# Performance work log

Measured on AMD Instinct MI355X. Metric: run time of the kernel, lower is better.

Reference implementation:

```python
import jax, jax.numpy as jnp
import numpy as np

MARGIN = 1.0
EPS = 1e-6  # torch F.pairwise_distance default eps, added elementwise to (x - y)
NEG_INF = -1e30
POS_INF = 1e30


def _pairwise_dist_matrix(e):
    # D[i,j] = || e_i - e_j + EPS ||_2, expanded so we never materialize [B,B,D]:
    # ||d + eps||^2 = ||d||^2 + 2*eps*sum(d) + Dfeat*eps^2,  d = e_i - e_j
    sq = jnp.sum(e * e, axis=1)          # [B]
    s = jnp.sum(e, axis=1)               # [B]
    d2 = (sq[:, None] + sq[None, :] - 2.0 * (e @ e.T)
          + 2.0 * EPS * (s[:, None] - s[None, :])
          + e.shape[1] * (EPS * EPS))
    return jnp.sqrt(jnp.maximum(d2, 0.0))  # [B,B]


def _pdist(x, y):
    # F.pairwise_distance(p=2): ||x - y + eps||
    return jnp.sqrt(jnp.sum(jnp.square(x - y + EPS), axis=-1))


def setup_inputs() -> dict:
    B, D = 4096, 128
    key = jax.random.key(0)
    k1, k2, k3, k4 = jax.random.split(key, 4)
    embedding = jax.random.normal(k1, (B, D), dtype=jnp.float32)
    # label space == batch, each label appears exactly once in the batch
    target_idx = jax.random.permutation(k2, B).astype(jnp.int32)
    positive_idxs = jax.random.bernoulli(k3, 0.02, (B, B))  # [B, L] label-space mask
    negative_idxs = jax.random.bernoulli(k4, 0.5, (B, B))
    return {"embedding": embedding, "target_idx": target_idx,
            "positive_idxs": positive_idxs, "negative_idxs": negative_idxs}


def reference(embedding, target_idx, positive_idxs, negative_idxs):
    # Mining happens under no_grad in the original module.
    dm = jax.lax.stop_gradient(_pairwise_dist_matrix(embedding))  # [B,B]
    # batch j is a positive/negative candidate for anchor i iff its label is flagged
    pos_mask = positive_idxs[:, target_idx]  # [B,B] bool
    neg_mask = negative_idxs[:, target_idx]
    pos_idx = jnp.argmax(jnp.where(pos_mask, dm, NEG_INF), axis=1)  # hardest positive
    neg_idx = jnp.argmin(jnp.where(neg_mask, dm, POS_INF), axis=1)  # hardest negative
    valid = jnp.any(pos_mask, axis=1) & jnp.any(neg_mask, axis=1)
    a = embedding
    p = embedding[pos_idx]
    n = embedding[neg_idx]
    ap = _pdist(a, p)
    an = _pdist(a, n)
    pn = _pdist(p, n)
    loss = jax.nn.relu(ap - jnp.minimum(an, pn) + MARGIN)
    w = valid.astype(loss.dtype)
    return jnp.sum(loss * w) / jnp.maximum(jnp.sum(w), 1.0)
```

## Files before the change

kernel.cpp:

```cpp
#include <hip/hip_runtime.h>
#include <stdint.h>

#define BN 4096
#define DD 128
#define EPSF 1e-6f
#define MARGINF 1.0f

typedef unsigned long long ull;
typedef unsigned short ushort;
typedef short short8 __attribute__((ext_vector_type(8)));
typedef float f32x4 __attribute__((ext_vector_type(4)));

__device__ __forceinline__ unsigned int ord_f32(float f) {
    unsigned int u = __float_as_uint(f);
    return (u & 0x80000000u) ? ~u : (u | 0x80000000u);
}
__device__ __forceinline__ ushort bf16_rne(float x) {
    unsigned int u = __float_as_uint(x);
    return (ushort)((u + 0x7FFFu + ((u >> 16) & 1u)) >> 16);
}

__global__ void k_prep(const float* __restrict__ e, const int* __restrict__ tidx,
                       float* __restrict__ rjp, unsigned int* __restrict__ jn,
                       ull* __restrict__ pk, ull* __restrict__ nk,
                       unsigned int* __restrict__ ehi, unsigned int* __restrict__ eperm) {
    int w = threadIdx.x >> 6, lane = threadIdx.x & 63;
    int row = blockIdx.x * 4 + w;
    int c = tidx[row];
    float2 v = ((const float2*)(e + (size_t)row * DD))[lane];
    ushort hx = bf16_rne(v.x), hy = bf16_rne(v.y);
    unsigned int packed = (unsigned int)hx | ((unsigned int)hy << 16);
    ehi[row * 64 + lane] = packed;
    eperm[(size_t)c * 64 + lane] = packed;
    float ss = v.x + v.y;
    float qq = v.x * v.x + v.y * v.y;
    #pragma unroll
    for (int off = 32; off > 0; off >>= 1) {
        ss += __shfl_down(ss, off);
        qq += __shfl_down(qq, off);
    }
    if (lane == 0) {
        rjp[c] = qq - 2.0f * EPSF * ss;
        jn[c] = 0xFFFFFFFFu - (unsigned int)row;
        pk[row] = 0ULL; nk[row] = 0ULL;
    }
}

__global__ __launch_bounds__(256, 4)
void k_select(const ushort* __restrict__ ehi, const ushort* __restrict__ eperm,
              const int* __restrict__ pos, const int* __restrict__ neg,
              const float* __restrict__ rjp, const unsigned int* __restrict__ jn,
              ull* __restrict__ pkey, ull* __restrict__ nkey) {
    __shared__ float rjL[1024];
    __shared__ unsigned int jnL[1024];
    __shared__ ull scrp[16 * 4], scrn[16 * 4];

    const int tid = threadIdx.x;
    const int lane = tid & 63, w = tid >> 6;
    const int lrow = lane & 15, quad = lane >> 4;
    const int r0 = blockIdx.x * 16;
    const int c0 = blockIdx.y * 1024;

    #pragma unroll
    for (int k = 0; k < 4; k++) {
        int idx = k * 256 + tid;
        rjL[idx] = rjp[c0 + idx];
        jnL[idx] = jn[c0 + idx];
    }

    short8 a[4];
    #pragma unroll
    for (int ks = 0; ks < 4; ks++)
        a[ks] = *(const short8*)(ehi + (size_t)(r0 + lrow) * DD + ks * 32 + quad * 8);

    __syncthreads();

    ull kp[4] = {0ULL, 0ULL, 0ULL, 0ULL};
    ull kn[4] = {0ULL, 0ULL, 0ULL, 0ULL};

    int pm[2][4], nm[2][4];
    short8 bf[2][4];
    float rjc[2]; unsigned int jni[2];

#define LOADTILE(BUF, JT) do {                                                 \
        const int lcol = (JT) * 64 + w * 16 + lrow;                            \
        rjc[BUF] = rjL[lcol];                                                  \
        jni[BUF] = jnL[lcol];                                                  \
        const int* pp = pos + (size_t)(r0 + quad * 4) * BN + (size_t)(c0 + lcol); \
        const int* np = neg + (size_t)(r0 + quad * 4) * BN + (size_t)(c0 + lcol); \
        _Pragma("unroll")                                                      \
        for (int t = 0; t < 4; t++) {                                          \
            pm[BUF][t] = __builtin_nontemporal_load(pp + (size_t)t * BN);      \
            nm[BUF][t] = __builtin_nontemporal_load(np + (size_t)t * BN);      \
        }                                                                      \
        const ushort* bp = eperm + (size_t)(c0 + lcol) * DD + quad * 8;        \
        _Pragma("unroll")                                                      \
        for (int ks = 0; ks < 4; ks++)                                         \
            bf[BUF][ks] = *(const short8*)(bp + ks * 32);                      \
    } while (0)

    LOADTILE(0, 0);

    #pragma unroll
    for (int jt = 0; jt < 16; jt++) {
        const int cur = jt & 1, nxt = cur ^ 1;
        if (jt < 15) {
            if (nxt == 0) LOADTILE(0, jt + 1); else LOADTILE(1, jt + 1);
        }
        f32x4 acc = (f32x4){0.f, 0.f, 0.f, 0.f};
        #pragma unroll
        for (int ks = 0; ks < 4; ks++)
            acc = __builtin_amdgcn_mfma_f32_16x16x32_bf16(a[ks], bf[cur][ks], acc, 0, 0, 0);
        #pragma unroll
        for (int t = 0; t < 4; t++) {
            float m = rjc[cur] - 2.0f * acc[t];
            unsigned int om = ord_f32(m);
            ull keyp = ((ull)om << 32) | (ull)jni[cur];
            ull keyn = ((ull)(om ^ 0xFFFFFFFFu) << 32) | (ull)jni[cur];
            if (pm[cur][t] != 0 && keyp > kp[t]) kp[t] = keyp;
            if (nm[cur][t] != 0 && keyn > kn[t]) kn[t] = keyn;
        }
    }
#undef LOADTILE

    #pragma unroll
    for (int t = 0; t < 4; t++) {
        #pragma unroll
        for (int off = 8; off > 0; off >>= 1) {
            ull o = __shfl_xor(kp[t], off); if (o > kp[t]) kp[t] = o;
            o = __shfl_xor(kn[t], off);     if (o > kn[t]) kn[t] = o;
        }
        if (lrow == 0) {
            scrp[(quad * 4 + t) * 4 + w] = kp[t];
            scrn[(quad * 4 + t) * 4 + w] = kn[t];
        }
    }
    __syncthreads();
    if (tid < 16) {
        ull xp = 0ULL, xn = 0ULL;
        #pragma unroll
        for (int k = 0; k < 4; k++) {
            ull v = scrp[tid * 4 + k]; if (v > xp) xp = v;
            v = scrn[tid * 4 + k];     if (v > xn) xn = v;
        }
        if (xp) atomicMax(&pkey[r0 + tid], xp);
        if (xn) atomicMax(&nkey[r0 + tid], xn);
    }
}

__global__ void k_loss(const float* __restrict__ e,
                       const ull* __restrict__ pkey, const ull* __restrict__ nkey,
                       float* __restrict__ partials) {
    int w = threadIdx.x >> 6, lane = threadIdx.x & 63;
    int row = blockIdx.x * 4 + w;
    ull pk = pkey[row], nk = nkey[row];
    float loss = 0.0f, wt = 0.0f;
    if (pk != 0ULL && nk != 0ULL) {
        int pi = (int)(0xFFFFFFFFu - (unsigned)(pk & 0xFFFFFFFFu));
        int ni = (int)(0xFFFFFFFFu - (unsigned)(nk & 0xFFFFFFFFu));
        float2 av = ((const float2*)(e + (size_t)row * DD))[lane];
        float2 pv = ((const float2*)(e + (size_t)pi * DD))[lane];
        float2 nv = ((const float2*)(e + (size_t)ni * DD))[lane];
        float dx, dy;
        dx = av.x - pv.x + EPSF; dy = av.y - pv.y + EPSF;
        float ap2 = dx * dx + dy * dy;
        dx = av.x - nv.x + EPSF; dy = av.y - nv.y + EPSF;
        float an2 = dx * dx + dy * dy;
        dx = pv.x - nv.x + EPSF; dy = pv.y - nv.y + EPSF;
        float pn2 = dx * dx + dy * dy;
        #pragma unroll
        for (int off = 32; off > 0; off >>= 1) {
            ap2 += __shfl_down(ap2, off);
            an2 += __shfl_down(an2, off);
            pn2 += __shfl_down(pn2, off);
        }
        if (lane == 0) {
            float ap = sqrtf(ap2), an = sqrtf(an2), pn = sqrtf(pn2);
            loss = fmaxf(ap - fminf(an, pn) + MARGINF, 0.0f);
            wt = 1.0f;
        }
    }
    __shared__ float sl[4], sw[4];
    if (lane == 0) { sl[w] = loss; sw[w] = wt; }
    __syncthreads();
    if (threadIdx.x == 0) {
        partials[blockIdx.x * 2 + 0] = sl[0] + sl[1] + sl[2] + sl[3];
        partials[blockIdx.x * 2 + 1] = sw[0] + sw[1] + sw[2] + sw[3];
    }
}

__global__ void k_final(const float* __restrict__ partials, float* __restrict__ out) {
    int tid = threadIdx.x;
    float L = 0.0f, W = 0.0f;
    for (int i = 0; i < 4; i++) {
        int idx = tid + i * 256;
        L += partials[idx * 2];
        W += partials[idx * 2 + 1];
    }
    #pragma unroll
    for (int off = 32; off > 0; off >>= 1) {
        L += __shfl_down(L, off);
        W += __shfl_down(W, off);
    }
    __shared__ float sl[4], sw[4];
    int w = tid >> 6, lane = tid & 63;
    if (lane == 0) { sl[w] = L; sw[w] = W; }
    __syncthreads();
    if (tid == 0) {
        float Lt = sl[0] + sl[1] + sl[2] + sl[3];
        float Wt = sw[0] + sw[1] + sw[2] + sw[3];
        out[0] = Lt / fmaxf(Wt, 1.0f);
    }
}

extern "C" void kernel_launch(void* const* d_in, const int* in_sizes, int n_in,
                              void* d_out, int out_size, void* d_ws, size_t ws_size,
                              hipStream_t stream) {
    const float* e    = (const float*)d_in[0];
    const int*   tidx = (const int*)d_in[1];
    const int*   pos  = (const int*)d_in[2];
    const int*   neg  = (const int*)d_in[3];
    float* out = (float*)d_out;

    ull* pkey  = (ull*)d_ws;
    ull* nkey  = pkey + BN;
    float* rjp = (float*)(nkey + BN);
    unsigned int* jn = (unsigned int*)(rjp + BN);
    float* partials  = (float*)(jn + BN);
    unsigned int* ehi   = (unsigned int*)(partials + 2048);
    unsigned int* eperm = ehi + (size_t)BN * 64;

    k_prep<<<BN / 4, 256, 0, stream>>>(e, tidx, rjp, jn, pkey, nkey, ehi, eperm);
    dim3 grid(BN / 16, 4);
    k_select<<<grid, 256, 0, stream>>>((const ushort*)ehi, (const ushort*)eperm,
                                       pos, neg, rjp, jn, pkey, nkey);
    k_loss<<<BN / 4, 256, 0, stream>>>(e, pkey, nkey, partials);
    k_final<<<1, 256, 0, stream>>>(partials, out);
}
```

Before: 184.5 us.

## Pack pos/neg int masks into bitmasks in prep kernel before selection

The prep kernel now streams each row of the int32 positive/negative masks with 16-byte nontemporal loads and packs them into 64-bit bitmasks. The selection kernel then reads one bit word per 64 columns instead of scattered int32 loads per element. The aim is better-coalesced mask streaming and fewer loads inside the MFMA loop. The cost is an extra 4 MB write and read, with the path gated on workspace size.

```diff
diff --git a/kernel.cpp b/kernel.cpp
--- a/kernel.cpp
+++ b/kernel.cpp
@@ -10,6 +10,7 @@
 typedef unsigned short ushort;
 typedef short short8 __attribute__((ext_vector_type(8)));
 typedef float f32x4 __attribute__((ext_vector_type(4)));
+typedef int int4v __attribute__((ext_vector_type(4)));
 
 __device__ __forceinline__ unsigned int ord_f32(float f) {
     unsigned int u = __float_as_uint(f);
@@ -20,13 +21,16 @@
     return (ushort)((u + 0x7FFFu + ((u >> 16) & 1u)) >> 16);
 }
 
+template<bool BITS>
 __global__ void k_prep(const float* __restrict__ e, const int* __restrict__ tidx,
+                       const int* __restrict__ pos, const int* __restrict__ neg,
                        float* __restrict__ rjp, unsigned int* __restrict__ jn,
-                       ull* __restrict__ pk, ull* __restrict__ nk,
-                       unsigned int* __restrict__ ehi, unsigned int* __restrict__ eperm) {
-    int w = threadIdx.x >> 6, lane = threadIdx.x & 63;
-    int row = blockIdx.x * 4 + w;
-    int c = tidx[row];
+                       ull* __restrict__ pkey, ull* __restrict__ nkey,
+                       unsigned int* __restrict__ ehi, unsigned int* __restrict__ eperm,
+                       ull* __restrict__ pbits, ull* __restrict__ nbits) {
+    const int w = threadIdx.x >> 6, lane = threadIdx.x & 63;
+    const int row = blockIdx.x * 4 + w;
+    const int c = tidx[row];
     float2 v = ((const float2*)(e + (size_t)row * DD))[lane];
     ushort hx = bf16_rne(v.x), hy = bf16_rne(v.y);
     unsigned int packed = (unsigned int)hx | ((unsigned int)hy << 16);
@@ -42,24 +46,51 @@
     if (lane == 0) {
         rjp[c] = qq - 2.0f * EPSF * ss;
         jn[c] = 0xFFFFFFFFu - (unsigned int)row;
-        pk[row] = 0ULL; nk[row] = 0ULL;
-    }
-}
-
+        pkey[row] = 0ULL; nkey[row] = 0ULL;
+    }
+    if (BITS) {
+        ushort* pb16 = (ushort*)pbits;
+        ushort* nb16 = (ushort*)nbits;
+        const int4v* prow = (const int4v*)(pos + (size_t)row * BN);
+        const int4v* nrow = (const int4v*)(neg + (size_t)row * BN);
+        #pragma unroll
+        for (int seg = 0; seg < 4; seg++) {
+            unsigned int pu = 0, nu = 0;
+            #pragma unroll
+            for (int k = 0; k < 4; k++) {
+                int4v P = __builtin_nontemporal_load(&prow[seg * 256 + lane * 4 + k]);
+                int4v N = __builtin_nontemporal_load(&nrow[seg * 256 + lane * 4 + k]);
+                unsigned int pq = (unsigned int)(P[0] != 0) | ((unsigned int)(P[1] != 0) << 1)
+                                | ((unsigned int)(P[2] != 0) << 2) | ((unsigned int)(P[3] != 0) << 3);
+                unsigned int nq = (unsigned int)(N[0] != 0) | ((unsigned int)(N[1] != 0) << 1)
+                                | ((unsigned int)(N[2] != 0) << 2) | ((unsigned int)(N[3] != 0) << 3);
+                pu |= pq << (4 * k);
+                nu |= nq << (4 * k);
+            }
+            pb16[row * 256 + seg * 64 + lane] = (ushort)pu;
+            nb16[row * 256 + seg * 64 + lane] = (ushort)nu;
+        }
+    }
+}
+
+template<bool BITS>
 __global__ __launch_bounds__(256, 4)
 void k_select(const ushort* __restrict__ ehi, const ushort* __restrict__ eperm,
               const int* __restrict__ pos, const int* __restrict__ neg,
+              const ull* __restrict__ pbits, const ull* __restrict__ nbits,
               const float* __restrict__ rjp, const unsigned int* __restrict__ jn,
               ull* __restrict__ pkey, ull* __restrict__ nkey) {
     __shared__ float rjL[1024];
     __shared__ unsigned int jnL[1024];
-    __shared__ ull scrp[16 * 4], scrn[16 * 4];
+    __shared__ ull scrp[64], scrn[64];
 
     const int tid = threadIdx.x;
     const int lane = tid & 63, w = tid >> 6;
     const int lrow = lane & 15, quad = lane >> 4;
     const int r0 = blockIdx.x * 16;
     const int c0 = blockIdx.y * 1024;
+    const int cb0 = c0 >> 6;
+    const int shft = w * 16 + lrow;
 
     #pragma unroll
     for (int k = 0; k < 4; k++) {
@@ -78,25 +109,36 @@
     ull kp[4] = {0ULL, 0ULL, 0ULL, 0ULL};
     ull kn[4] = {0ULL, 0ULL, 0ULL, 0ULL};
 
+    ull pmw[2][4], nmw[2][4];
     int pm[2][4], nm[2][4];
     short8 bf[2][4];
     float rjc[2]; unsigned int jni[2];
 
-#define LOADTILE(BUF, JT) do {                                                 \
-        const int lcol = (JT) * 64 + w * 16 + lrow;                            \
-        rjc[BUF] = rjL[lcol];                                                  \
-        jni[BUF] = jnL[lcol];                                                  \
-        const int* pp = pos + (size_t)(r0 + quad * 4) * BN + (size_t)(c0 + lcol); \
-        const int* np = neg + (size_t)(r0 + quad * 4) * BN + (size_t)(c0 + lcol); \
-        _Pragma("unroll")                                                      \
-        for (int t = 0; t < 4; t++) {                                          \
-            pm[BUF][t] = __builtin_nontemporal_load(pp + (size_t)t * BN);      \
-            nm[BUF][t] = __builtin_nontemporal_load(np + (size_t)t * BN);      \
-        }                                                                      \
-        const ushort* bp = eperm + (size_t)(c0 + lcol) * DD + quad * 8;        \
-        _Pragma("unroll")                                                      \
-        for (int ks = 0; ks < 4; ks++)                                         \
-            bf[BUF][ks] = *(const short8*)(bp + ks * 32);                      \
+#define LOADTILE(BUF, JT) do {                                                  \
+        const int lcol = (JT) * 64 + shft;                                      \
+        rjc[BUF] = rjL[lcol];                                                   \
+        jni[BUF] = jnL[lcol];                                                   \
+        if (BITS) {                                                             \
+            const ull* pb = pbits + (size_t)(r0 + quad * 4) * 64 + cb0 + (JT);  \
+            const ull* nb = nbits + (size_t)(r0 + quad * 4) * 64 + cb0 + (JT);  \
+            _Pragma("unroll")                                                   \
+            for (int t = 0; t < 4; t++) {                                       \
+                pmw[BUF][t] = pb[(size_t)t * 64];                               \
+                nmw[BUF][t] = nb[(size_t)t * 64];                               \
+            }                                                                   \
+        } else {                                                                \
+            const int* pp = pos + (size_t)(r0 + quad * 4) * BN + (size_t)(c0 + lcol); \
+            const int* np = neg + (size_t)(r0 + quad * 4) * BN + (size_t)(c0 + lcol); \
+            _Pragma("unroll")                                                   \
+            for (int t = 0; t < 4; t++) {                                       \
+                pm[BUF][t] = __builtin_nontemporal_load(pp + (size_t)t * BN);   \
+                nm[BUF][t] = __builtin_nontemporal_load(np + (size_t)t * BN);   \
+            }                                                                   \
+        }                                                                       \
+        const ushort* bp = eperm + (size_t)(c0 + lcol) * DD + quad * 8;         \
+        _Pragma("unroll")                                                       \
+        for (int ks = 0; ks < 4; ks++)                                          \
+            bf[BUF][ks] = *(const short8*)(bp + ks * 32);                       \
     } while (0)
 
     LOADTILE(0, 0);
@@ -117,8 +159,10 @@
             unsigned int om = ord_f32(m);
             ull keyp = ((ull)om << 32) | (ull)jni[cur];
             ull keyn = ((ull)(om ^ 0xFFFFFFFFu) << 32) | (ull)jni[cur];
-            if (pm[cur][t] != 0 && keyp > kp[t]) kp[t] = keyp;
-            if (nm[cur][t] != 0 && keyn > kn[t]) kn[t] = keyn;
+            bool pok = BITS ? (((pmw[cur][t] >> shft) & 1ULL) != 0ULL) : (pm[cur][t] != 0);
+            bool nok = BITS ? (((nmw[cur][t] >> shft) & 1ULL) != 0ULL) : (nm[cur][t] != 0);
+            if (pok && keyp > kp[t]) kp[t] = keyp;
+            if (nok && keyn > kn[t]) kn[t] = keyn;
         }
     }
 #undef LOADTILE
@@ -222,18 +266,33 @@
     const int*   neg  = (const int*)d_in[3];
     float* out = (float*)d_out;
 
-    ull* pkey  = (ull*)d_ws;
-    ull* nkey  = pkey + BN;
-    float* rjp = (float*)(nkey + BN);
-    unsigned int* jn = (unsigned int*)(rjp + BN);
-    float* partials  = (float*)(jn + BN);
-    unsigned int* ehi   = (unsigned int*)(partials + 2048);
-    unsigned int* eperm = ehi + (size_t)BN * 64;
-
-    k_prep<<<BN / 4, 256, 0, stream>>>(e, tidx, rjp, jn, pkey, nkey, ehi, eperm);
+    char* p = (char*)d_ws;
+    ull* pkey  = (ull*)p;                 p += (size_t)BN * 8;
+    ull* nkey  = (ull*)p;                 p += (size_t)BN * 8;
+    float* rjp = (float*)p;               p += (size_t)BN * 4;
+    unsigned int* jn = (unsigned int*)p;  p += (size_t)BN * 4;
+    float* partials = (float*)p;          p += 2048 * 4;
+    unsigned int* ehi = (unsigned int*)p; p += (size_t)BN * 64 * 4;
+    unsigned int* eperm = (unsigned int*)p; p += (size_t)BN * 64 * 4;
+    ull* pbits = (ull*)p;                 p += (size_t)BN * 64 * 8;
+    ull* nbits = (ull*)p;                 p += (size_t)BN * 64 * 8;
+    const size_t need = (size_t)(p - (char*)d_ws);
+    const bool bits = ws_size >= need;
+
     dim3 grid(BN / 16, 4);
-    k_select<<<grid, 256, 0, stream>>>((const ushort*)ehi, (const ushort*)eperm,
-                                       pos, neg, rjp, jn, pkey, nkey);
+    if (bits) {
+        k_prep<true><<<BN / 4, 256, 0, stream>>>(e, tidx, pos, neg, rjp, jn,
+                                                 pkey, nkey, ehi, eperm, pbits, nbits);
+        k_select<true><<<grid, 256, 0, stream>>>((const ushort*)ehi, (const ushort*)eperm,
+                                                 pos, neg, pbits, nbits,
+                                                 rjp, jn, pkey, nkey);
+    } else {
+        k_prep<false><<<BN / 4, 256, 0, stream>>>(e, tidx, pos, neg, rjp, jn,
+                                                  pkey, nkey, ehi, eperm, pbits, nbits);
+        k_select<false><<<grid, 256, 0, stream>>>((const ushort*)ehi, (const ushort*)eperm,
+                                                  pos, neg, pbits, nbits,
+                                                  rjp, jn, pkey, nkey);
+    }
     k_loss<<<BN / 4, 256, 0, stream>>>(e, pkey, nkey, partials);
     k_final<<<1, 256, 0, stream>>>(partials, out);
 }
```

Measured after the change: 213.7 us. 1.16x slower.
